# Kernel optimization log

Hardware: AMD Instinct MI355X
Metric: run time of the kernel (lower is better)

## Reference

```python
import jax, jax.numpy as jnp
import numpy as np

NUM_BINS = 32
SIGMA_RATIO = 1.0
SMOOTH_NR = 1e-7
SMOOTH_DR = 1e-7


def _parzen_weights(x, bin_centers, preterm):
    # x: [B, N]; returns normalized Gaussian Parzen weights [B, N, K]
    d = x[..., None] - bin_centers  # [B, N, K]
    w = jnp.exp(-preterm * d * d)
    return w / jnp.sum(w, axis=-1, keepdims=True)


def _mi_loss(pred, target):
    B = pred.shape[0]
    p = pred.reshape(B, -1)  # [B, N]
    t = target.reshape(B, -1)
    N = p.shape[1]

    # min/max are detached (.item() in torch); images in [0,1] use fixed range (0,1)
    minval = jax.lax.stop_gradient(jnp.minimum(p.min(), t.min()))
    maxval = jax.lax.stop_gradient(jnp.maximum(p.max(), t.max()))
    in_range = (maxval <= 1.0) & (minval >= 0.0)
    minval = jnp.where(in_range, jnp.float32(0.0), minval)
    maxval = jnp.where(in_range, jnp.float32(1.0), maxval)

    bin_centers = minval + (maxval - minval) * jnp.linspace(0.0, 1.0, NUM_BINS, dtype=p.dtype)  # [K]
    sigma = (maxval - minval) / (NUM_BINS - 1) * SIGMA_RATIO
    preterm = 1.0 / (2.0 * sigma * sigma)

    wa = _parzen_weights(p, bin_centers, preterm)  # [B, N, K]
    wb = _parzen_weights(t, bin_centers, preterm)  # [B, N, K]

    pa = jnp.mean(wa, axis=1)  # [B, K] == pa of shape B,1,K squeezed
    pb = jnp.mean(wb, axis=1)  # [B, K]
    pab = jnp.einsum('bnk,bnl->bkl', wa, wb) / N  # [B, K, K] joint histogram
    papb = pa[:, :, None] * pb[:, None, :]  # [B, K, K] outer product == bmm(pa^T, pb)

    mi = jnp.sum(pab * jnp.log((pab + SMOOTH_NR) / (papb + SMOOTH_DR) + SMOOTH_DR), axis=(-1, -2))  # [B]
    return -jnp.mean(mi)  # reduction='mean', negated


def setup_inputs() -> dict:
    key = jax.random.key(0)
    k1, k2 = jax.random.split(key)
    shape = (1, 1, 128, 128, 128)
    pred = jax.random.uniform(k1, shape, dtype=jnp.float32)
    target = jax.random.uniform(k2, shape, dtype=jnp.float32)
    return {"pred": pred, "target": target}


def reference(pred, target):
    return _mi_loss(pred, target)
```

## Files before the change

kernel.cpp:

```cpp
#include <hip/hip_runtime.h>
#include <math.h>

#ifndef __has_builtin
#define __has_builtin(x) 0
#endif
#if __has_builtin(__builtin_amdgcn_exp2f)
#define EXP2F(x) __builtin_amdgcn_exp2f(x)
#else
#define EXP2F(x) exp2f(x)
#endif
#if __has_builtin(__builtin_amdgcn_rcpf)
#define RCPF(x) __builtin_amdgcn_rcpf(x)
#else
#define RCPF(x) (1.0f / (x))
#endif

typedef _Float16 f16x8 __attribute__((ext_vector_type(8)));
typedef float f32x4 __attribute__((ext_vector_type(4)));

constexpr int KBINS = 32;
constexpr int MM_BLOCKS = 512;
constexpr int MAIN_BLOCKS = 1024;
constexpr int WAVES_PER_BLOCK = 4;
constexpr int BATCH = 32;
constexpr int RED_BLOCKS = 64;
constexpr int PART_OFF_F = 4096;
constexpr size_t REDA_OFF_B = (size_t)(PART_OFF_F + MAIN_BLOCKS * KBINS * KBINS) * 4;
constexpr float WSCALE = 512.0f;

#define MFMA16(a, b, c) __builtin_amdgcn_mfma_f32_16x16x32_f16((a), (b), (c), 0, 0, 0)

template <int CTRL>
__device__ __forceinline__ float rot_add(float v) {
  int r = __builtin_amdgcn_update_dpp(0, __builtin_bit_cast(int, v), CTRL, 0xF, 0xF, true);
  return v + __builtin_bit_cast(float, r);
}
__device__ __forceinline__ float row_sum16(float v) {
  v = rot_add<0x128>(v);
  v = rot_add<0x124>(v);
  v = rot_add<0x122>(v);
  v = rot_add<0x121>(v);
  return v;
}

__global__ __launch_bounds__(256) void k_minmax(const float* __restrict__ p,
                                                const float* __restrict__ t,
                                                int n, float* __restrict__ ws) {
  int tid = blockIdx.x * 256 + threadIdx.x;
  int nth = gridDim.x * 256;
  float mn = INFINITY, mx = -INFINITY;
  int n4 = n >> 2;
  const float4* p4 = (const float4*)p;
  const float4* t4 = (const float4*)t;
  for (int i = tid; i < n4; i += nth) {
    float4 a = p4[i];
    mn = fminf(mn, fminf(fminf(a.x, a.y), fminf(a.z, a.w)));
    mx = fmaxf(mx, fmaxf(fmaxf(a.x, a.y), fmaxf(a.z, a.w)));
    float4 b = t4[i];
    mn = fminf(mn, fminf(fminf(b.x, b.y), fminf(b.z, b.w)));
    mx = fmaxf(mx, fmaxf(fmaxf(b.x, b.y), fmaxf(b.z, b.w)));
  }
  for (int i = (n4 << 2) + tid; i < n; i += nth) {
    mn = fminf(mn, fminf(p[i], t[i]));
    mx = fmaxf(mx, fmaxf(p[i], t[i]));
  }
  for (int off = 32; off; off >>= 1) {
    mn = fminf(mn, __shfl_xor(mn, off, 64));
    mx = fmaxf(mx, __shfl_xor(mx, off, 64));
  }
  __shared__ float smn[4], smx[4];
  int wv = threadIdx.x >> 6;
  if ((threadIdx.x & 63) == 0) { smn[wv] = mn; smx[wv] = mx; }
  __syncthreads();
  if (threadIdx.x == 0) {
    mn = fminf(fminf(smn[0], smn[1]), fminf(smn[2], smn[3]));
    mx = fmaxf(fmaxf(smx[0], smx[1]), fmaxf(smx[2], smx[3]));
    ws[16 + 2 * blockIdx.x] = mn;
    ws[17 + 2 * blockIdx.x] = mx;
  }
}

__global__ __launch_bounds__(256, 4) void k_main(const float* __restrict__ p,
                                                 const float* __restrict__ t,
                                                 int n, float* __restrict__ ws) {
  __shared__ float s_par[4];
  __shared__ float red[WAVES_PER_BLOCK][KBINS * KBINS];

  const int tidx = threadIdx.x;
  const int lane = tidx & 63;
  const int wv = tidx >> 6;

  if (tidx < 64) {
    float mn = INFINITY, mx = -INFINITY;
    for (int b = lane; b < MM_BLOCKS; b += 64) {
      mn = fminf(mn, ws[16 + 2 * b]);
      mx = fmaxf(mx, ws[17 + 2 * b]);
    }
    for (int off = 32; off; off >>= 1) {
      mn = fminf(mn, __shfl_xor(mn, off, 64));
      mx = fmaxf(mx, __shfl_xor(mx, off, 64));
    }
    if (lane == 0) {
      bool in_range = (mx <= 1.0f) && (mn >= 0.0f);
      float minv = in_range ? 0.0f : mn;
      float maxv = in_range ? 1.0f : mx;
      float drange = maxv - minv;
      float sigma = drange * (1.0f / (KBINS - 1));
      float preterm = 1.0f / (2.0f * sigma * sigma);
      s_par[0] = minv;
      s_par[1] = drange * (1.0f / (KBINS - 1));
      s_par[2] = preterm * 1.44269504088896340736f;
    }
  }
  __syncthreads();
  const float minv = s_par[0], delta = s_par[1];
  const float npl2 = -s_par[2];

  const int m = lane & 15;
  const int quad = lane >> 4;
  const int qb = quad << 3;
  const float c0 = fmaf(delta, (float)m, minv);
  const float c1 = fmaf(delta, (float)(m + 16), minv);

  f32x4 acc00 = {0.f, 0.f, 0.f, 0.f};
  f32x4 acc01 = {0.f, 0.f, 0.f, 0.f};
  f32x4 acc10 = {0.f, 0.f, 0.f, 0.f};
  f32x4 acc11 = {0.f, 0.f, 0.f, 0.f};

  const int per_wave = n >> 12;
  const int base = (blockIdx.x * WAVES_PER_BLOCK + wv) * per_wave;
  const int li = lane & 31;
  const float* __restrict__ src = (lane & 32) ? t : p;
  const int loff = (lane & 32) ? base - 32 : base;

  for (int it = 0; it < per_wave; it += BATCH) {
    float xv = src[loff + it + lane - (lane & 32) + (lane & 32 ? 32 : 0)];
    xv = src[base + it + li];

    f16x8 Ah0, Al0, Ah1, Al1, Bh0, Bl0, Bh1, Bl1;
#pragma unroll
    for (int j = 0; j < 8; ++j) {
      float xa = __shfl(xv, qb + j, 64);
      float xb = __shfl(xv, 32 + qb + j, 64);
      {
        float d0 = xa - c0, d1 = xa - c1;
        float e0 = EXP2F((npl2 * d0) * d0);
        float e1 = EXP2F((npl2 * d1) * d1);
        float s = row_sum16(e0 + e1);
        float inv = RCPF(s);
        inv = inv * fmaf(-s, inv, 2.0f);
        inv *= WSCALE;
        float w0 = e0 * inv, w1 = e1 * inv;
        _Float16 h0 = (_Float16)w0;
        _Float16 l0 = (_Float16)(w0 - (float)h0);
        _Float16 h1 = (_Float16)w1;
        _Float16 l1 = (_Float16)(w1 - (float)h1);
        Ah0[j] = h0; Al0[j] = l0; Ah1[j] = h1; Al1[j] = l1;
      }
      {
        float d0 = xb - c0, d1 = xb - c1;
        float e0 = EXP2F((npl2 * d0) * d0);
        float e1 = EXP2F((npl2 * d1) * d1);
        float s = row_sum16(e0 + e1);
        float inv = RCPF(s);
        inv = inv * fmaf(-s, inv, 2.0f);
        inv *= WSCALE;
        float w0 = e0 * inv, w1 = e1 * inv;
        _Float16 h0 = (_Float16)w0;
        _Float16 l0 = (_Float16)(w0 - (float)h0);
        _Float16 h1 = (_Float16)w1;
        _Float16 l1 = (_Float16)(w1 - (float)h1);
        Bh0[j] = h0; Bl0[j] = l0; Bh1[j] = h1; Bl1[j] = l1;
      }
    }

    acc00 = MFMA16(Ah0, Bh0, acc00);
    acc01 = MFMA16(Ah0, Bh1, acc01);
    acc10 = MFMA16(Ah1, Bh0, acc10);
    acc11 = MFMA16(Ah1, Bh1, acc11);
    acc00 = MFMA16(Al0, Bh0, acc00);
    acc01 = MFMA16(Al0, Bh1, acc01);
    acc10 = MFMA16(Al1, Bh0, acc10);
    acc11 = MFMA16(Al1, Bh1, acc11);
    acc00 = MFMA16(Ah0, Bl0, acc00);
    acc01 = MFMA16(Ah0, Bl1, acc01);
    acc10 = MFMA16(Ah1, Bl0, acc10);
    acc11 = MFMA16(Ah1, Bl1, acc11);
    acc00 = MFMA16(Al0, Bl0, acc00);
    acc01 = MFMA16(Al0, Bl1, acc01);
    acc10 = MFMA16(Al1, Bl0, acc10);
    acc11 = MFMA16(Al1, Bl1, acc11);
  }

#pragma unroll
  for (int reg = 0; reg < 4; ++reg) {
    int r0 = quad * 4 + reg;
    red[wv][r0 * KBINS + m] = acc00[reg];
    red[wv][r0 * KBINS + 16 + m] = acc01[reg];
    red[wv][(16 + r0) * KBINS + m] = acc10[reg];
    red[wv][(16 + r0) * KBINS + 16 + m] = acc11[reg];
  }
  __syncthreads();

  int cell = tidx * 4;
  float4 out4;
  out4.x = (red[0][cell + 0] + red[1][cell + 0]) + (red[2][cell + 0] + red[3][cell + 0]);
  out4.y = (red[0][cell + 1] + red[1][cell + 1]) + (red[2][cell + 1] + red[3][cell + 1]);
  out4.z = (red[0][cell + 2] + red[1][cell + 2]) + (red[2][cell + 2] + red[3][cell + 2]);
  out4.w = (red[0][cell + 3] + red[1][cell + 3]) + (red[2][cell + 3] + red[3][cell + 3]);
  float4* part = (float4*)(ws + PART_OFF_F + (size_t)blockIdx.x * 1024);
  part[tidx] = out4;
}

__global__ __launch_bounds__(1024) void k_reduceA(float* __restrict__ ws) {
  const float* part = ws + PART_OFF_F;
  double* outp = (double*)((char*)ws + REDA_OFF_B);
  int tid = threadIdx.x;
  int r = blockIdx.x;
  double s = 0.0;
#pragma unroll
  for (int b = 0; b < MAIN_BLOCKS / RED_BLOCKS; ++b)
    s += (double)part[(size_t)(r * (MAIN_BLOCKS / RED_BLOCKS) + b) * 1024 + tid];
  outp[(size_t)r * 1024 + tid] = s;
}

__global__ __launch_bounds__(1024) void k_final(const float* __restrict__ ws_f,
                                                float* __restrict__ out, int n) {
  const double* parts = (const double*)((const char*)ws_f + REDA_OFF_B);
  __shared__ double pab_s[1024];
  __shared__ double pa_s[32], pb_s[32];
  __shared__ double wsum[16];
  int tid = threadIdx.x;
  double s = 0.0;
#pragma unroll 8
  for (int r = 0; r < RED_BLOCKS; ++r) s += parts[(size_t)r * 1024 + tid];
  double pab = s / ((double)n * 262144.0);
  pab_s[tid] = pab;
  __syncthreads();
  if (tid < 32) {
    double a = 0.0;
    for (int l = 0; l < 32; ++l) a += pab_s[tid * 32 + l];
    pa_s[tid] = a;
  } else if (tid < 64) {
    int l = tid - 32;
    double b = 0.0;
    for (int k2 = 0; k2 < 32; ++k2) b += pab_s[k2 * 32 + l];
    pb_s[l] = b;
  }
  __syncthreads();
  int k = tid >> 5, l = tid & 31;
  double papb = pa_s[k] * pb_s[l];
  double v = pab * log((pab + 1e-7) / (papb + 1e-7) + 1e-7);
  for (int off = 32; off; off >>= 1) v += __shfl_down(v, off, 64);
  if ((tid & 63) == 0) wsum[tid >> 6] = v;
  __syncthreads();
  if (tid < 64) {
    double w = (tid < 16) ? wsum[tid] : 0.0;
    for (int off = 8; off; off >>= 1) w += __shfl_down(w, off, 64);
    if (tid == 0) out[0] = (float)(-w);
  }
}

extern "C" void kernel_launch(void* const* d_in, const int* in_sizes, int n_in,
                              void* d_out, int out_size, void* d_ws, size_t ws_size,
                              hipStream_t stream) {
  const float* p = (const float*)d_in[0];
  const float* t = (const float*)d_in[1];
  float* out = (float*)d_out;
  float* ws = (float*)d_ws;
  int n = in_sizes[0];

  k_minmax<<<dim3(MM_BLOCKS), dim3(256), 0, stream>>>(p, t, n, ws);
  k_main<<<dim3(MAIN_BLOCKS), dim3(256), 0, stream>>>(p, t, n, ws);
  k_reduceA<<<dim3(RED_BLOCKS), dim3(1024), 0, stream>>>(ws);
  k_final<<<dim3(1), dim3(1024), 0, stream>>>(ws, out, n);
}
```

Before: 139.1 us.

## Load inputs as float4 per lane, pack fp16 with cvt_pkrtz, use 8-wave blocks

Each lane now loads its own 8 pred and 8 target values with float4 loads, replacing the per-element cross-lane shuffles. Weight conversion to fp16 hi/lo pairs uses the packed round-toward-zero convert instruction. The exponent gets a +9 bias folded into the FMA, which cancels in the normalisation. Blocks grow to 512 threads (8 waves), so each wave handles half as many elements and the final per-block reduction sums 8 wave partials. The 512-thread launch bound with min 4 blocks tightens the register budget and could force spills. Rounding toward zero shifts the hi/lo split slightly, though the lo term absorbs the residual.

```diff
diff --git a/kernel.cpp b/kernel.cpp
--- a/kernel.cpp
+++ b/kernel.cpp
@@ -16,12 +16,28 @@
 #endif
 
 typedef _Float16 f16x8 __attribute__((ext_vector_type(8)));
+typedef _Float16 h2 __attribute__((ext_vector_type(2)));
 typedef float f32x4 __attribute__((ext_vector_type(4)));
+
+union Frag {
+  f16x8 v;
+  h2 p[4];
+  _Float16 e[8];
+};
+
+__device__ __forceinline__ h2 pkrtz(float a, float b) {
+#if __has_builtin(__builtin_amdgcn_cvt_pkrtz)
+  return __builtin_bit_cast(h2, __builtin_amdgcn_cvt_pkrtz(a, b));
+#else
+  h2 r; r.x = (_Float16)a; r.y = (_Float16)b; return r;
+#endif
+}
 
 constexpr int KBINS = 32;
 constexpr int MM_BLOCKS = 512;
 constexpr int MAIN_BLOCKS = 1024;
-constexpr int WAVES_PER_BLOCK = 4;
+constexpr int NTHR = 512;
+constexpr int WPB = 8;
 constexpr int BATCH = 32;
 constexpr int RED_BLOCKS = 64;
 constexpr int PART_OFF_F = 4096;
@@ -41,6 +57,19 @@
   v = rot_add<0x122>(v);
   v = rot_add<0x121>(v);
   return v;
+}
+
+__device__ __forceinline__ void wpair(float x, float c0, float c1, float npl2,
+                                      float& w0, float& w1) {
+  float d0 = x - c0, d1 = x - c1;
+  float e0 = EXP2F(fmaf(npl2 * d0, d0, 9.0f));
+  float e1 = EXP2F(fmaf(npl2 * d1, d1, 9.0f));
+  float s = row_sum16(e0 + e1);
+  float inv = RCPF(s);
+  inv = inv * fmaf(-s, inv, 2.0f);
+  inv *= WSCALE;
+  w0 = e0 * inv;
+  w1 = e1 * inv;
 }
 
 __global__ __launch_bounds__(256) void k_minmax(const float* __restrict__ p,
@@ -80,11 +109,11 @@
   }
 }
 
-__global__ __launch_bounds__(256, 4) void k_main(const float* __restrict__ p,
-                                                 const float* __restrict__ t,
-                                                 int n, float* __restrict__ ws) {
+__global__ __launch_bounds__(NTHR, 4) void k_main(const float* __restrict__ p,
+                                                  const float* __restrict__ t,
+                                                  int n, float* __restrict__ ws) {
+  __shared__ __align__(16) float red[WPB][KBINS * KBINS];
   __shared__ float s_par[4];
-  __shared__ float red[WAVES_PER_BLOCK][KBINS * KBINS];
 
   const int tidx = threadIdx.x;
   const int lane = tidx & 63;
@@ -127,69 +156,60 @@
   f32x4 acc10 = {0.f, 0.f, 0.f, 0.f};
   f32x4 acc11 = {0.f, 0.f, 0.f, 0.f};
 
-  const int per_wave = n >> 12;
-  const int base = (blockIdx.x * WAVES_PER_BLOCK + wv) * per_wave;
-  const int li = lane & 31;
-  const float* __restrict__ src = (lane & 32) ? t : p;
-  const int loff = (lane & 32) ? base - 32 : base;
+  const int per_wave = n >> 13;
+  const int base = (blockIdx.x * WPB + wv) * per_wave;
 
   for (int it = 0; it < per_wave; it += BATCH) {
-    float xv = src[loff + it + lane - (lane & 32) + (lane & 32 ? 32 : 0)];
-    xv = src[base + it + li];
-
-    f16x8 Ah0, Al0, Ah1, Al1, Bh0, Bl0, Bh1, Bl1;
-#pragma unroll
-    for (int j = 0; j < 8; ++j) {
-      float xa = __shfl(xv, qb + j, 64);
-      float xb = __shfl(xv, 32 + qb + j, 64);
+    const int sbase = base + it + qb;
+    float4 a0 = *(const float4*)(p + sbase);
+    float4 a1 = *(const float4*)(p + sbase + 4);
+    float4 b0 = *(const float4*)(t + sbase);
+    float4 b1 = *(const float4*)(t + sbase + 4);
+    float xa[8] = {a0.x, a0.y, a0.z, a0.w, a1.x, a1.y, a1.z, a1.w};
+    float xb[8] = {b0.x, b0.y, b0.z, b0.w, b1.x, b1.y, b1.z, b1.w};
+
+    Frag Ah0, Al0, Ah1, Al1, Bh0, Bl0, Bh1, Bl1;
+#pragma unroll
+    for (int jp = 0; jp < 4; ++jp) {
       {
-        float d0 = xa - c0, d1 = xa - c1;
-        float e0 = EXP2F((npl2 * d0) * d0);
-        float e1 = EXP2F((npl2 * d1) * d1);
-        float s = row_sum16(e0 + e1);
-        float inv = RCPF(s);
-        inv = inv * fmaf(-s, inv, 2.0f);
-        inv *= WSCALE;
-        float w0 = e0 * inv, w1 = e1 * inv;
-        _Float16 h0 = (_Float16)w0;
-        _Float16 l0 = (_Float16)(w0 - (float)h0);
-        _Float16 h1 = (_Float16)w1;
-        _Float16 l1 = (_Float16)(w1 - (float)h1);
-        Ah0[j] = h0; Al0[j] = l0; Ah1[j] = h1; Al1[j] = l1;
+        float w00, w10, w01, w11;
+        wpair(xa[2 * jp], c0, c1, npl2, w00, w10);
+        wpair(xa[2 * jp + 1], c0, c1, npl2, w01, w11);
+        h2 h0 = pkrtz(w00, w01);
+        h2 h1 = pkrtz(w10, w11);
+        Ah0.p[jp] = h0;
+        Ah1.p[jp] = h1;
+        Al0.p[jp] = pkrtz(w00 - (float)h0.x, w01 - (float)h0.y);
+        Al1.p[jp] = pkrtz(w10 - (float)h1.x, w11 - (float)h1.y);
       }
       {
-        float d0 = xb - c0, d1 = xb - c1;
-        float e0 = EXP2F((npl2 * d0) * d0);
-        float e1 = EXP2F((npl2 * d1) * d1);
-        float s = row_sum16(e0 + e1);
-        float inv = RCPF(s);
-        inv = inv * fmaf(-s, inv, 2.0f);
-        inv *= WSCALE;
-        float w0 = e0 * inv, w1 = e1 * inv;
-        _Float16 h0 = (_Float16)w0;
-        _Float16 l0 = (_Float16)(w0 - (float)h0);
-        _Float16 h1 = (_Float16)w1;
-        _Float16 l1 = (_Float16)(w1 - (float)h1);
-        Bh0[j] = h0; Bl0[j] = l0; Bh1[j] = h1; Bl1[j] = l1;
+        float w00, w10, w01, w11;
+        wpair(xb[2 * jp], c0, c1, npl2, w00, w10);
+        wpair(xb[2 * jp + 1], c0, c1, npl2, w01, w11);
+        h2 h0 = pkrtz(w00, w01);
+        h2 h1 = pkrtz(w10, w11);
+        Bh0.p[jp] = h0;
+        Bh1.p[jp] = h1;
+        Bl0.p[jp] = pkrtz(w00 - (float)h0.x, w01 - (float)h0.y);
+        Bl1.p[jp] = pkrtz(w10 - (float)h1.x, w11 - (float)h1.y);
       }
     }
-
-    acc00 = MFMA16(Ah0, Bh0, acc00);
-    acc01 = MFMA16(Ah0, Bh1, acc01);
-    acc10 = MFMA16(Ah1, Bh0, acc10);
-    acc11 = MFMA16(Ah1, Bh1, acc11);
-    acc00 = MFMA16(Al0, Bh0, acc00);
-    acc01 = MFMA16(Al0, Bh1, acc01);
-    acc10 = MFMA16(Al1, Bh0, acc10);
-    acc11 = MFMA16(Al1, Bh1, acc11);
-    acc00 = MFMA16(Ah0, Bl0, acc00);
-    acc01 = MFMA16(Ah0, Bl1, acc01);
-    acc10 = MFMA16(Ah1, Bl0, acc10);
-    acc11 = MFMA16(Ah1, Bl1, acc11);
-    acc00 = MFMA16(Al0, Bl0, acc00);
-    acc01 = MFMA16(Al0, Bl1, acc01);
-    acc10 = MFMA16(Al1, Bl0, acc10);
-    acc11 = MFMA16(Al1, Bl1, acc11);
+    acc00 = MFMA16(Ah0.v, Bh0.v, acc00);
+    acc01 = MFMA16(Ah0.v, Bh1.v, acc01);
+    acc10 = MFMA16(Ah1.v, Bh0.v, acc10);
+    acc11 = MFMA16(Ah1.v, Bh1.v, acc11);
+    acc00 = MFMA16(Al0.v, Bh0.v, acc00);
+    acc01 = MFMA16(Al0.v, Bh1.v, acc01);
+    acc10 = MFMA16(Al1.v, Bh0.v, acc10);
+    acc11 = MFMA16(Al1.v, Bh1.v, acc11);
+    acc00 = MFMA16(Ah0.v, Bl0.v, acc00);
+    acc01 = MFMA16(Ah0.v, Bl1.v, acc01);
+    acc10 = MFMA16(Ah1.v, Bl0.v, acc10);
+    acc11 = MFMA16(Ah1.v, Bl1.v, acc11);
+    acc00 = MFMA16(Al0.v, Bl0.v, acc00);
+    acc01 = MFMA16(Al0.v, Bl1.v, acc01);
+    acc10 = MFMA16(Al1.v, Bl0.v, acc10);
+    acc11 = MFMA16(Al1.v, Bl1.v, acc11);
   }
 
 #pragma unroll
@@ -201,15 +221,17 @@
     red[wv][(16 + r0) * KBINS + 16 + m] = acc11[reg];
   }
   __syncthreads();
-
-  int cell = tidx * 4;
-  float4 out4;
-  out4.x = (red[0][cell + 0] + red[1][cell + 0]) + (red[2][cell + 0] + red[3][cell + 0]);
-  out4.y = (red[0][cell + 1] + red[1][cell + 1]) + (red[2][cell + 1] + red[3][cell + 1]);
-  out4.z = (red[0][cell + 2] + red[1][cell + 2]) + (red[2][cell + 2] + red[3][cell + 2]);
-  out4.w = (red[0][cell + 3] + red[1][cell + 3]) + (red[2][cell + 3] + red[3][cell + 3]);
-  float4* part = (float4*)(ws + PART_OFF_F + (size_t)blockIdx.x * 1024);
-  part[tidx] = out4;
+  {
+    int c = 2 * tidx;
+    float s0 = 0.f, s1 = 0.f;
+#pragma unroll
+    for (int w = 0; w < WPB; ++w) {
+      float2 v = *(const float2*)&red[w][c];
+      s0 += v.x;
+      s1 += v.y;
+    }
+    *(float2*)(ws + PART_OFF_F + (size_t)blockIdx.x * 1024 + c) = make_float2(s0, s1);
+  }
 }
 
 __global__ __launch_bounds__(1024) void k_reduceA(float* __restrict__ ws) {
@@ -271,7 +293,7 @@
   int n = in_sizes[0];
 
   k_minmax<<<dim3(MM_BLOCKS), dim3(256), 0, stream>>>(p, t, n, ws);
-  k_main<<<dim3(MAIN_BLOCKS), dim3(256), 0, stream>>>(p, t, n, ws);
+  k_main<<<dim3(MAIN_BLOCKS), dim3(NTHR), 0, stream>>>(p, t, n, ws);
   k_reduceA<<<dim3(RED_BLOCKS), dim3(1024), 0, stream>>>(ws);
   k_final<<<dim3(1), dim3(1024), 0, stream>>>(ws, out, n);
 }
```

Result: faster. 130.2 us (-6.4%).
